# Performance work log

Measured on AMD Instinct MI355X. Metric: run time of the kernel, lower is better.

The kernel has to match this reference:

```python
import jax, jax.numpy as jnp
import numpy as np

BN_EPS = 1e-5

def _bn_relu(x, gamma, beta):
    # x: [E, B, F]; BatchNorm1d in training mode: batch stats over B, biased var
    mu = jnp.mean(x, axis=1, keepdims=True)
    var = jnp.mean(jnp.square(x - mu), axis=1, keepdims=True)
    y = gamma[:, None, :] * (x - mu) * jax.lax.rsqrt(var + BN_EPS) + beta[:, None, :]
    return jax.nn.relu(y)

def setup_inputs() -> dict:
    key = jax.random.key(0)
    ks = jax.random.split(key, 4)
    B, D, E, H1, H2, T = 32768, 1472, 8, 512, 256, 2
    s1 = (2.0 / D) ** 0.5
    s2 = (2.0 / H1) ** 0.5
    return {
        "x_deep": jax.random.normal(ks[0], (B, D), jnp.float32),
        "W1": jax.random.normal(ks[1], (E, D, H1), jnp.float32) * s1,
        "b1": jnp.zeros((E, H1), jnp.float32),
        "g1": jnp.ones((E, H1), jnp.float32),
        "be1": jnp.zeros((E, H1), jnp.float32),
        "W2": jax.random.normal(ks[2], (E, H1, H2), jnp.float32) * s2,
        "b2": jnp.zeros((E, H2), jnp.float32),
        "g2": jnp.ones((E, H2), jnp.float32),
        "be2": jnp.zeros((E, H2), jnp.float32),
        "Wg": jax.random.normal(ks[3], (T, D, E), jnp.float32) * s1,
        "bg": jnp.zeros((T, E), jnp.float32),
    }

def reference(x_deep, W1, b1, g1, be1, W2, b2, g2, be2, Wg, bg):
    # Experts: batched over expert dim E (replaces Python loop over nn.ModuleList)
    h = jnp.einsum('bd,edh->ebh', x_deep, W1) + b1[:, None, :]   # [E,B,H1]
    h = _bn_relu(h, g1, be1)                                     # dropout: identity (eval)
    h = jnp.einsum('ebh,ehk->ebk', h, W2) + b2[:, None, :]       # [E,B,H2]
    experts_out = _bn_relu(h, g2, be2)                           # [E,B,H2]
    # Gates: [T,B,E], softmax over experts
    gates = jax.nn.softmax(jnp.einsum('bd,tde->tbe', x_deep, Wg) + bg[:, None, :], axis=-1)
    # Combine: task_out[t] = reshape(experts_out * gate[...,None], [B, E*H2])
    task = experts_out[None, :, :, :] * jnp.transpose(gates, (0, 2, 1))[:, :, :, None]  # [T,E,B,H2]
    T, E, B, H2 = task.shape
    out = jnp.transpose(task, (0, 2, 1, 3)).reshape(T, B, E * H2)  # [T,B,E*H2]
    return out
```

## Files before the change

### kernel.cpp

```cpp
#include <hip/hip_runtime.h>
#include <cstdint>


typedef __attribute__((ext_vector_type(8))) __bf16 bf16x8;
typedef __attribute__((ext_vector_type(4))) float f32x4;

__device__ __forceinline__ unsigned short f2bf(float f) {
  unsigned int u = __float_as_uint(f);
  u += 0x7fffu + ((u >> 16) & 1u);
  return (unsigned short)(u >> 16);
}

__device__ __forceinline__ void async16(const void* g, void* l) {
  __builtin_amdgcn_global_load_lds((__attribute__((address_space(1))) unsigned int*)g,
                                   (__attribute__((address_space(3))) unsigned int*)l,
                                   16, 0, 0);
}

__global__ void convert_f32_bf16(const float* __restrict__ in,
                                 unsigned short* __restrict__ out, size_t n) {
  size_t i = ((size_t)blockIdx.x * blockDim.x + threadIdx.x) * 4;
  if (i + 3 < n) {
    float4 v = *(const float4*)(in + i);
    unsigned int w0 = (unsigned int)f2bf(v.x) | ((unsigned int)f2bf(v.y) << 16);
    unsigned int w1 = (unsigned int)f2bf(v.z) | ((unsigned int)f2bf(v.w) << 16);
    *(uint2*)(out + i) = make_uint2(w0, w1);
  }
}

__global__ void transpose_bf16(const float* __restrict__ W,
                               unsigned short* __restrict__ Wt, int D, int H) {
  __shared__ float tile[32][33];
  int e = blockIdx.z;
  int d0 = blockIdx.x * 32, h0 = blockIdx.y * 32;
  const float* We = W + (size_t)e * D * H;
  unsigned short* Wte = Wt + (size_t)e * D * H;
  int tx = threadIdx.x, ty = threadIdx.y;
#pragma unroll
  for (int i = 0; i < 4; ++i)
    tile[ty + i * 8][tx] = We[(size_t)(d0 + ty + i * 8) * H + h0 + tx];
  __syncthreads();
#pragma unroll
  for (int i = 0; i < 4; ++i)
    Wte[(size_t)(h0 + ty + i * 8) * D + d0 + tx] = f2bf(tile[tx][ty + i * 8]);
}

__global__ void transpose_wg(const float* __restrict__ Wg,
                             unsigned short* __restrict__ Wt, int D) {
  int idx = blockIdx.x * 256 + threadIdx.x;
  int te = idx / D, d = idx - te * D;
  int t = te >> 3, e = te & 7;
  Wt[(size_t)te * D + d] = f2bf(Wg[((size_t)t * D + d) * 8 + e]);
}

__global__ __launch_bounds__(512, 2) void gemm256(
    const unsigned short* __restrict__ A, int lda,
    const unsigned short* __restrict__ Bt,
    unsigned short* __restrict__ C, int ldc, int K,
    size_t aStrideE, size_t bStrideE, size_t cStrideE,
    float* __restrict__ sum, float* __restrict__ sq,
    int statStrideE, int statCols, int groupM, int GN) {
  __shared__ __attribute__((aligned(128))) char smem[131072];
  const int tid = threadIdx.x;
  const int lane = tid & 63;
  const int wid = tid >> 6;
  const int wm = wid & 1;
  const int wn = wid >> 1;
  const int e = blockIdx.z;

  int bx, by;
  if (groupM) {
    int bid = blockIdx.x;
    int cpx = (int)gridDim.x >> 3;
    int b2 = (bid & 7) * cpx + (bid >> 3);
    int gsize = groupM * GN;
    int gid = b2 / gsize;
    int rem = b2 - gid * gsize;
    bx = gid * groupM + rem % groupM;
    by = rem / groupM;
  } else {
    bx = blockIdx.x; by = blockIdx.y;
  }

  const unsigned short* Ae = A + (size_t)e * aStrideE + (size_t)bx * 256 * lda;
  const unsigned short* Be = Bt + (size_t)e * bStrideE + (size_t)by * 256 * K;

  const int srow = tid >> 2;
  const int scol = 8 * ((tid & 3) ^ ((tid >> 3) & 3));
  const unsigned short* gA = Ae + (size_t)srow * lda + scol;
  const unsigned short* gB = Be + (size_t)srow * K + scol;
  const size_t aRow128 = (size_t)128 * lda;
  const size_t bRow128 = (size_t)128 * K;
  char* ldsDst = smem + tid * 16;

  auto stageA = [&](int u) {
    char* d = ldsDst + (u & 3) * 32768;
    const unsigned short* g = gA + u * 32;
    async16(g, d);
    async16(g + aRow128, d + 8192);
  };
  auto stageB = [&](int u) {
    char* d = ldsDst + (u & 3) * 32768 + 16384;
    const unsigned short* g = gB + u * 32;
    async16(g, d);
    async16(g + bRow128, d + 8192);
  };

  const int mrow = lane & 15;
  const int kgb = ((lane >> 4) << 4) ^ (((mrow >> 1) & 3) << 4);
  const char* rdA = smem + (wm * 128 + mrow) * 64 + kgb;
  const char* rdB = smem + 16384 + (wn * 64 + mrow) * 64 + kgb;

  f32x4 acc[8][4] = {};
  const int NS = K >> 5;

  auto slab = [&](int u, bool st) {
    const char* pa = rdA + (u & 3) * 32768;
    const char* pb = rdB + (u & 3) * 32768;
    bf16x8 af[4], bfr[4];
#pragma unroll
    for (int i = 0; i < 4; ++i) af[i] = *(const bf16x8*)(pa + i * 1024);
#pragma unroll
    for (int j = 0; j < 4; ++j) bfr[j] = *(const bf16x8*)(pb + j * 1024);
    if (st) stageA(u + 2);
    __builtin_amdgcn_s_barrier();
    __builtin_amdgcn_s_setprio(1);
#pragma unroll
    for (int i = 0; i < 4; ++i)
#pragma unroll
      for (int j = 0; j < 4; ++j)
        acc[i][j] = __builtin_amdgcn_mfma_f32_16x16x32_bf16(af[i], bfr[j], acc[i][j], 0, 0, 0);
    __builtin_amdgcn_s_setprio(0);
    __builtin_amdgcn_s_barrier();
#pragma unroll
    for (int i = 0; i < 4; ++i) af[i] = *(const bf16x8*)(pa + (i + 4) * 1024);
    if (st) stageB(u + 2);
    __builtin_amdgcn_s_barrier();
    __builtin_amdgcn_s_setprio(1);
#pragma unroll
    for (int i = 0; i < 4; ++i)
#pragma unroll
      for (int j = 0; j < 4; ++j)
        acc[i + 4][j] = __builtin_amdgcn_mfma_f32_16x16x32_bf16(af[i], bfr[j], acc[i + 4][j], 0, 0, 0);
    __builtin_amdgcn_s_setprio(0);
  };

  stageA(0); stageB(0); stageA(1); stageB(1);
  asm volatile("s_waitcnt vmcnt(4)");
  __builtin_amdgcn_s_barrier();
  __builtin_amdgcn_sched_barrier(0);

  int u = 0;
  for (; u < NS - 2; ++u) {
    slab(u, true);
    asm volatile("s_waitcnt vmcnt(4)");
    __builtin_amdgcn_s_barrier();
    __builtin_amdgcn_sched_barrier(0);
  }
  slab(u, false); ++u;
  asm volatile("s_waitcnt vmcnt(0)");
  __builtin_amdgcn_s_barrier();
  __builtin_amdgcn_sched_barrier(0);
  slab(u, false);

  unsigned short* Ce = C + (size_t)e * cStrideE + (size_t)bx * 256 * ldc +
                       (size_t)by * 256;
  const int r0 = wm * 128 + (lane >> 4) * 4;
  const int c0 = wn * 64 + mrow;
#pragma unroll
  for (int i = 0; i < 8; ++i)
#pragma unroll
    for (int j = 0; j < 4; ++j)
#pragma unroll
      for (int r = 0; r < 4; ++r)
        Ce[(size_t)(r0 + i * 16 + r) * ldc + c0 + j * 16] = f2bf(acc[i][j][r]);

  float* se = sum + (size_t)e * statStrideE;
  float* qe = sq + (size_t)e * statStrideE;
#pragma unroll
  for (int j = 0; j < 4; ++j) {
    float s = 0.f, q = 0.f;
#pragma unroll
    for (int i = 0; i < 8; ++i)
#pragma unroll
      for (int r = 0; r < 4; ++r) {
        float v = acc[i][j][r];
        s += v;
        q = fmaf(v, v, q);
      }
    s += __shfl_xor(s, 16, 64); s += __shfl_xor(s, 32, 64);
    q += __shfl_xor(q, 16, 64); q += __shfl_xor(q, 32, 64);
    if ((lane >> 4) == 0) {
      int col = by * 256 + wn * 64 + j * 16 + mrow;
      if (col < statCols) {
        atomicAdd(&se[col], s);
        atomicAdd(&qe[col], q);
      }
    }
  }
}

__global__ void bn_coef(const float* __restrict__ sum, const float* __restrict__ sq,
                        const float* __restrict__ g, const float* __restrict__ be,
                        float* __restrict__ A, float* __restrict__ C, int n, float invB) {
  int i = blockIdx.x * blockDim.x + threadIdx.x;
  if (i < n) {
    float mean = sum[i] * invB;
    float var = sq[i] * invB - mean * mean;
    float a = g[i] * rsqrtf(var + 1e-5f);
    A[i] = a;
    C[i] = be[i] - mean * a;
  }
}

__global__ __launch_bounds__(256) void gates_mfma(
    const unsigned short* __restrict__ xb,
    const unsigned short* __restrict__ wgt,
    const float* __restrict__ bg,
    float* __restrict__ gates, int Bn) {
  const int lane = threadIdx.x & 63;
  const int w = threadIdx.x >> 6;
  const int row0 = blockIdx.x * 64 + w * 16;
  const int mrow = lane & 15, kseg = (lane >> 4) * 8;
  const unsigned short* pa = xb + (size_t)(row0 + mrow) * 1472 + kseg;
  const unsigned short* pb = wgt + (size_t)mrow * 1472 + kseg;
  f32x4 acc = {};
  bf16x8 a0 = *(const bf16x8*)pa, b0 = *(const bf16x8*)pb;
  for (int ks = 1; ks < 46; ++ks) {
    bf16x8 a1 = *(const bf16x8*)(pa + ks * 32);
    bf16x8 b1 = *(const bf16x8*)(pb + ks * 32);
    acc = __builtin_amdgcn_mfma_f32_16x16x32_bf16(a0, b0, acc, 0, 0, 0);
    a0 = a1; b0 = b1;
  }
  acc = __builtin_amdgcn_mfma_f32_16x16x32_bf16(a0, b0, acc, 0, 0, 0);
  const int c = lane & 15;
  const float bias = bg[c];
#pragma unroll
  for (int r = 0; r < 4; ++r) {
    float v = acc[r] + bias;
    float m = v;
    m = fmaxf(m, __shfl_xor(m, 1, 64));
    m = fmaxf(m, __shfl_xor(m, 2, 64));
    m = fmaxf(m, __shfl_xor(m, 4, 64));
    float p = expf(v - m);
    float s = p;
    s += __shfl_xor(s, 1, 64);
    s += __shfl_xor(s, 2, 64);
    s += __shfl_xor(s, 4, 64);
    int rowg = row0 + (lane >> 4) * 4 + r;
    gates[((size_t)(c >> 3) * Bn + rowg) * 8 + (c & 7)] = p / s;
  }
}

__global__ void bn_relu_inplace(unsigned short* __restrict__ h, const float* __restrict__ A,
                                const float* __restrict__ C) {
  int tid = blockIdx.x * blockDim.x + threadIdx.x;
  int r = tid >> 9, cb = tid & 511;
  int col = cb * 8;
  size_t i = (size_t)r * 4096 + col;
  uint4 v = *(const uint4*)(h + i);
  unsigned int w[4] = {v.x, v.y, v.z, v.w};
#pragma unroll
  for (int j = 0; j < 4; ++j) {
    float f0 = __uint_as_float(w[j] << 16);
    float f1 = __uint_as_float(w[j] & 0xffff0000u);
    float y0 = fmaxf(fmaf(A[col + 2 * j], f0, C[col + 2 * j]), 0.f);
    float y1 = fmaxf(fmaf(A[col + 2 * j + 1], f1, C[col + 2 * j + 1]), 0.f);
    w[j] = (unsigned int)f2bf(y0) | ((unsigned int)f2bf(y1) << 16);
  }
  *(uint4*)(h + i) = make_uint4(w[0], w[1], w[2], w[3]);
}

__global__ void combine(const unsigned short* __restrict__ h2,
                        const float* __restrict__ A, const float* __restrict__ C,
                        const float* __restrict__ gates,
                        float* __restrict__ out, int Bn) {
  int b = blockIdx.x;
  int c = threadIdx.x * 8;
  int e = c >> 8;
  uint4 v = *(const uint4*)(h2 + (size_t)b * 2048 + c);
  unsigned int w[4] = {v.x, v.y, v.z, v.w};
  float y[8];
#pragma unroll
  for (int j = 0; j < 4; ++j) {
    float f0 = __uint_as_float(w[j] << 16);
    float f1 = __uint_as_float(w[j] & 0xffff0000u);
    y[2 * j]     = fmaxf(fmaf(A[c + 2 * j], f0, C[c + 2 * j]), 0.f);
    y[2 * j + 1] = fmaxf(fmaf(A[c + 2 * j + 1], f1, C[c + 2 * j + 1]), 0.f);
  }
  float g0 = gates[(size_t)b * 8 + e];
  float g1 = gates[((size_t)Bn + b) * 8 + e];
  float4* o0 = (float4*)(out + (size_t)b * 2048 + c);
  float4* o1 = (float4*)(out + ((size_t)Bn + b) * 2048 + c);
  o0[0] = make_float4(y[0] * g0, y[1] * g0, y[2] * g0, y[3] * g0);
  o0[1] = make_float4(y[4] * g0, y[5] * g0, y[6] * g0, y[7] * g0);
  o1[0] = make_float4(y[0] * g1, y[1] * g1, y[2] * g1, y[3] * g1);
  o1[1] = make_float4(y[4] * g1, y[5] * g1, y[6] * g1, y[7] * g1);
}

extern "C" void kernel_launch(void* const* d_in, const int* in_sizes, int n_in,
                              void* d_out, int out_size, void* d_ws, size_t ws_size,
                              hipStream_t stream) {
  const int B = 32768, D = 1472, E = 8, H1 = 512, H2 = 256;
  const int N1 = E * H1;
  const float* x   = (const float*)d_in[0];
  const float* W1  = (const float*)d_in[1];
  const float* g1  = (const float*)d_in[3];
  const float* be1 = (const float*)d_in[4];
  const float* W2  = (const float*)d_in[5];
  const float* g2  = (const float*)d_in[7];
  const float* be2 = (const float*)d_in[8];
  const float* Wg  = (const float*)d_in[9];
  const float* bg  = (const float*)d_in[10];
  float* out = (float*)d_out;

  char* p = (char*)d_ws;
  unsigned short* x_b = (unsigned short*)p; p += (size_t)B * D * 2;
  unsigned short* W1t = (unsigned short*)p; p += (size_t)N1 * D * 2;
  unsigned short* Wgt = (unsigned short*)p; p += (size_t)16 * D * 2;
  unsigned short* W2t = (unsigned short*)p; p += (size_t)E * H2 * H1 * 2;
  unsigned short* h1b = (unsigned short*)p; p += (size_t)B * N1 * 2;
  unsigned short* h2b = (unsigned short*)p; p += (size_t)B * E * H2 * 2;
  float* gatesBuf = (float*)p; p += (size_t)2 * B * 8 * 4;
  float* sum1 = (float*)p; p += (size_t)N1 * 4;
  float* sq1  = (float*)p; p += (size_t)N1 * 4;
  float* sum2 = (float*)p; p += (size_t)E * H2 * 4;
  float* sq2  = (float*)p; p += (size_t)E * H2 * 4;
  float* A1   = (float*)p; p += (size_t)N1 * 4;
  float* C1   = (float*)p; p += (size_t)N1 * 4;
  float* A2   = (float*)p; p += (size_t)E * H2 * 4;
  float* C2   = (float*)p; p += (size_t)E * H2 * 4;

  hipMemsetAsync(sum1, 0, (size_t)(2 * N1 + 2 * E * H2) * 4, stream);

  convert_f32_bf16<<<(unsigned)((size_t)B * D / 1024), 256, 0, stream>>>(
      x, x_b, (size_t)B * D);
  transpose_bf16<<<dim3(D / 32, H1 / 32, E), dim3(32, 8), 0, stream>>>(W1, W1t, D, H1);
  transpose_wg<<<16 * D / 256, 256, 0, stream>>>(Wg, Wgt, D);
  transpose_bf16<<<dim3(H1 / 32, H2 / 32, E), dim3(32, 8), 0, stream>>>(W2, W2t, H1, H2);

  gemm256<<<dim3(128 * 16), 512, 0, stream>>>(
      x_b, D, W1t, h1b, N1, D, (size_t)0, (size_t)0, (size_t)0,
      sum1, sq1, 0, N1, 16, 16);

  bn_coef<<<N1 / 256, 256, 0, stream>>>(sum1, sq1, g1, be1, A1, C1, N1, 1.f / B);
  gates_mfma<<<B / 64, 256, 0, stream>>>(x_b, Wgt, bg, gatesBuf, B);
  bn_relu_inplace<<<(unsigned)((size_t)B * 512 / 256), 256, 0, stream>>>(h1b, A1, C1);

  gemm256<<<dim3(B / 256, 1, E), 512, 0, stream>>>(
      h1b, N1, W2t, h2b, E * H2, H1,
      (size_t)H1, (size_t)H1 * H2, (size_t)H2,
      sum2, sq2, H2, H2, 0, 0);

  bn_coef<<<E * H2 / 256, 256, 0, stream>>>(sum2, sq2, g2, be2, A2, C2, E * H2, 1.f / B);

  combine<<<B, 256, 0, stream>>>(h2b, A2, C2, gatesBuf, out, B);
}
```

Before: 1.458 ms.

## Fuse BN1+ReLU into second expert GEMM's A-operand load path

Removes the separate in-place BN+ReLU pass over the 32768x4096 bf16 hidden activation and applies the affine+ReLU while staging A tiles into LDS in a new dedicated GEMM2 kernel with a double-buffered register-load pipeline. This saves a full read and write of h1. The new kernel uses a shallower 2-stage pipeline with synchronous register loads for A instead of the 4-stage async pipeline, which may expose more memory latency. The generic GEMM loses its per-expert stride parameters.

Measured after the change: 1.351 ms. -7.4%, faster.

```diff
diff --git a/kernel.cpp b/kernel.cpp
--- a/kernel.cpp
+++ b/kernel.cpp
@@ -57,33 +57,26 @@
     const unsigned short* __restrict__ A, int lda,
     const unsigned short* __restrict__ Bt,
     unsigned short* __restrict__ C, int ldc, int K,
-    size_t aStrideE, size_t bStrideE, size_t cStrideE,
     float* __restrict__ sum, float* __restrict__ sq,
-    int statStrideE, int statCols, int groupM, int GN) {
+    int statCols, int groupM, int GN) {
   __shared__ __attribute__((aligned(128))) char smem[131072];
   const int tid = threadIdx.x;
   const int lane = tid & 63;
   const int wid = tid >> 6;
   const int wm = wid & 1;
   const int wn = wid >> 1;
-  const int e = blockIdx.z;
-
-  int bx, by;
-  if (groupM) {
-    int bid = blockIdx.x;
-    int cpx = (int)gridDim.x >> 3;
-    int b2 = (bid & 7) * cpx + (bid >> 3);
-    int gsize = groupM * GN;
-    int gid = b2 / gsize;
-    int rem = b2 - gid * gsize;
-    bx = gid * groupM + rem % groupM;
-    by = rem / groupM;
-  } else {
-    bx = blockIdx.x; by = blockIdx.y;
-  }
-
-  const unsigned short* Ae = A + (size_t)e * aStrideE + (size_t)bx * 256 * lda;
-  const unsigned short* Be = Bt + (size_t)e * bStrideE + (size_t)by * 256 * K;
+
+  int bid = blockIdx.x;
+  int cpx = (int)gridDim.x >> 3;
+  int b2 = (bid & 7) * cpx + (bid >> 3);
+  int gsize = groupM * GN;
+  int gid = b2 / gsize;
+  int rem = b2 - gid * gsize;
+  int bx = gid * groupM + rem % groupM;
+  int by = rem / groupM;
+
+  const unsigned short* Ae = A + (size_t)bx * 256 * lda;
+  const unsigned short* Be = Bt + (size_t)by * 256 * K;
 
   const int srow = tid >> 2;
   const int scol = 8 * ((tid & 3) ^ ((tid >> 3) & 3));
@@ -163,8 +156,7 @@
   __builtin_amdgcn_sched_barrier(0);
   slab(u, false);
 
-  unsigned short* Ce = C + (size_t)e * cStrideE + (size_t)bx * 256 * ldc +
-                       (size_t)by * 256;
+  unsigned short* Ce = C + (size_t)bx * 256 * ldc + (size_t)by * 256;
   const int r0 = wm * 128 + (lane >> 4) * 4;
   const int c0 = wn * 64 + mrow;
 #pragma unroll
@@ -175,8 +167,6 @@
       for (int r = 0; r < 4; ++r)
         Ce[(size_t)(r0 + i * 16 + r) * ldc + c0 + j * 16] = f2bf(acc[i][j][r]);
 
-  float* se = sum + (size_t)e * statStrideE;
-  float* qe = sq + (size_t)e * statStrideE;
 #pragma unroll
   for (int j = 0; j < 4; ++j) {
     float s = 0.f, q = 0.f;
@@ -193,9 +183,136 @@
     if ((lane >> 4) == 0) {
       int col = by * 256 + wn * 64 + j * 16 + mrow;
       if (col < statCols) {
-        atomicAdd(&se[col], s);
-        atomicAdd(&qe[col], q);
+        atomicAdd(&sum[col], s);
+        atomicAdd(&sq[col], q);
       }
+    }
+  }
+}
+
+__global__ __launch_bounds__(512) void gemm2_fused(
+    const unsigned short* __restrict__ H1,
+    const float* __restrict__ A1, const float* __restrict__ C1,
+    const unsigned short* __restrict__ W2t,
+    unsigned short* __restrict__ H2,
+    float* __restrict__ sum, float* __restrict__ sq) {
+  __shared__ __attribute__((aligned(128))) char smem[2][32768];
+  const int tid = threadIdx.x;
+  const int lane = tid & 63;
+  const int wid = tid >> 6;
+  const int wm = wid & 1;
+  const int wn = wid >> 1;
+  const int e = blockIdx.z;
+  const int bx = blockIdx.x;
+
+  const unsigned short* Ae = H1 + (size_t)bx * 256 * 4096 + e * 512;
+  const unsigned short* Be = W2t + (size_t)e * 256 * 512;
+
+  const int srow = tid >> 2;
+  const int scol = 8 * ((tid & 3) ^ ((tid >> 3) & 3));
+  const unsigned short* gA = Ae + (size_t)srow * 4096 + scol;
+  const unsigned short* gB = Be + (size_t)srow * 512 + scol;
+  const size_t aRow128 = (size_t)128 * 4096;
+  const size_t bRow128 = (size_t)128 * 512;
+  const float* a1p = A1 + e * 512 + scol;
+  const float* c1p = C1 + e * 512 + scol;
+
+  auto bnrelu = [&](uint4 v, int kc) -> uint4 {
+    unsigned int w[4] = {v.x, v.y, v.z, v.w};
+    unsigned int o[4];
+#pragma unroll
+    for (int j = 0; j < 4; ++j) {
+      float f0 = __uint_as_float(w[j] << 16);
+      float f1 = __uint_as_float(w[j] & 0xffff0000u);
+      float y0 = fmaxf(fmaf(a1p[kc + 2 * j], f0, c1p[kc + 2 * j]), 0.f);
+      float y1 = fmaxf(fmaf(a1p[kc + 2 * j + 1], f1, c1p[kc + 2 * j + 1]), 0.f);
+      o[j] = (unsigned int)f2bf(y0) | ((unsigned int)f2bf(y1) << 16);
+    }
+    return make_uint4(o[0], o[1], o[2], o[3]);
+  };
+
+  const int mrow = lane & 15;
+  const int kgb = ((lane >> 4) << 4) ^ (((mrow >> 1) & 3) << 4);
+  const int rdAo = (wm * 128 + mrow) * 64 + kgb;
+  const int rdBo = 16384 + (wn * 64 + mrow) * 64 + kgb;
+
+  f32x4 acc[8][4] = {};
+
+  {
+    uint4 va0 = *(const uint4*)(gA);
+    uint4 va1 = *(const uint4*)(gA + aRow128);
+    async16(gB, smem[0] + tid * 16 + 16384);
+    async16(gB + bRow128, smem[0] + tid * 16 + 16384 + 8192);
+    uint4 t0 = bnrelu(va0, 0), t1 = bnrelu(va1, 0);
+    *(uint4*)(smem[0] + tid * 16) = t0;
+    *(uint4*)(smem[0] + tid * 16 + 8192) = t1;
+  }
+  __syncthreads();
+
+  for (int u = 0; u < 16; ++u) {
+    const int slot = u & 1, nslot = slot ^ 1;
+    uint4 va0, va1;
+    if (u < 15) {
+      va0 = *(const uint4*)(gA + (u + 1) * 32);
+      va1 = *(const uint4*)(gA + (u + 1) * 32 + aRow128);
+      async16(gB + (u + 1) * 32, smem[nslot] + tid * 16 + 16384);
+      async16(gB + (u + 1) * 32 + bRow128, smem[nslot] + tid * 16 + 16384 + 8192);
+    }
+    {
+      const char* pa = smem[slot] + rdAo;
+      const char* pb = smem[slot] + rdBo;
+      bf16x8 af[8], bfr[4];
+#pragma unroll
+      for (int i = 0; i < 8; ++i) af[i] = *(const bf16x8*)(pa + i * 1024);
+#pragma unroll
+      for (int j = 0; j < 4; ++j) bfr[j] = *(const bf16x8*)(pb + j * 1024);
+      __builtin_amdgcn_s_setprio(1);
+#pragma unroll
+      for (int i = 0; i < 8; ++i)
+#pragma unroll
+        for (int j = 0; j < 4; ++j)
+          acc[i][j] = __builtin_amdgcn_mfma_f32_16x16x32_bf16(af[i], bfr[j], acc[i][j], 0, 0, 0);
+      __builtin_amdgcn_s_setprio(0);
+    }
+    if (u < 15) {
+      uint4 t0 = bnrelu(va0, (u + 1) * 32);
+      uint4 t1 = bnrelu(va1, (u + 1) * 32);
+      *(uint4*)(smem[nslot] + tid * 16) = t0;
+      *(uint4*)(smem[nslot] + tid * 16 + 8192) = t1;
+    }
+    __syncthreads();
+  }
+
+  unsigned short* Ce = H2 + (size_t)bx * 256 * 2048 + e * 256;
+  const int r0 = wm * 128 + (lane >> 4) * 4;
+  const int c0 = wn * 64 + mrow;
+#pragma unroll
+  for (int i = 0; i < 8; ++i)
+#pragma unroll
+    for (int j = 0; j < 4; ++j)
+#pragma unroll
+      for (int r = 0; r < 4; ++r)
+        Ce[(size_t)(r0 + i * 16 + r) * 2048 + c0 + j * 16] = f2bf(acc[i][j][r]);
+
+  float* se = sum + (size_t)e * 256;
+  float* qe = sq + (size_t)e * 256;
+#pragma unroll
+  for (int j = 0; j < 4; ++j) {
+    float s = 0.f, q = 0.f;
+#pragma unroll
+    for (int i = 0; i < 8; ++i)
+#pragma unroll
+      for (int r = 0; r < 4; ++r) {
+        float v = acc[i][j][r];
+        s += v;
+        q = fmaf(v, v, q);
+      }
+    s += __shfl_xor(s, 16, 64); s += __shfl_xor(s, 32, 64);
+    q += __shfl_xor(q, 16, 64); q += __shfl_xor(q, 32, 64);
+    if ((lane >> 4) == 0) {
+      int col = wn * 64 + j * 16 + mrow;
+      atomicAdd(&se[col], s);
+      atomicAdd(&qe[col], q);
     }
   }
 }
@@ -252,25 +369,6 @@
   }
 }
 
-__global__ void bn_relu_inplace(unsigned short* __restrict__ h, const float* __restrict__ A,
-                                const float* __restrict__ C) {
-  int tid = blockIdx.x * blockDim.x + threadIdx.x;
-  int r = tid >> 9, cb = tid & 511;
-  int col = cb * 8;
-  size_t i = (size_t)r * 4096 + col;
-  uint4 v = *(const uint4*)(h + i);
-  unsigned int w[4] = {v.x, v.y, v.z, v.w};
-#pragma unroll
-  for (int j = 0; j < 4; ++j) {
-    float f0 = __uint_as_float(w[j] << 16);
-    float f1 = __uint_as_float(w[j] & 0xffff0000u);
-    float y0 = fmaxf(fmaf(A[col + 2 * j], f0, C[col + 2 * j]), 0.f);
-    float y1 = fmaxf(fmaf(A[col + 2 * j + 1], f1, C[col + 2 * j + 1]), 0.f);
-    w[j] = (unsigned int)f2bf(y0) | ((unsigned int)f2bf(y1) << 16);
-  }
-  *(uint4*)(h + i) = make_uint4(w[0], w[1], w[2], w[3]);
-}
-
 __global__ void combine(const unsigned short* __restrict__ h2,
                         const float* __restrict__ A, const float* __restrict__ C,
                         const float* __restrict__ gates,
@@ -340,17 +438,13 @@
   transpose_bf16<<<dim3(H1 / 32, H2 / 32, E), dim3(32, 8), 0, stream>>>(W2, W2t, H1, H2);
 
   gemm256<<<dim3(128 * 16), 512, 0, stream>>>(
-      x_b, D, W1t, h1b, N1, D, (size_t)0, (size_t)0, (size_t)0,
-      sum1, sq1, 0, N1, 16, 16);
+      x_b, D, W1t, h1b, N1, D, sum1, sq1, N1, 16, 16);
 
   bn_coef<<<N1 / 256, 256, 0, stream>>>(sum1, sq1, g1, be1, A1, C1, N1, 1.f / B);
   gates_mfma<<<B / 64, 256, 0, stream>>>(x_b, Wgt, bg, gatesBuf, B);
-  bn_relu_inplace<<<(unsigned)((size_t)B * 512 / 256), 256, 0, stream>>>(h1b, A1, C1);
-
-  gemm256<<<dim3(B / 256, 1, E), 512, 0, stream>>>(
-      h1b, N1, W2t, h2b, E * H2, H1,
-      (size_t)H1, (size_t)H1 * H2, (size_t)H2,
-      sum2, sq2, H2, H2, 0, 0);
+
+  gemm2_fused<<<dim3(B / 256, 1, E), 512, 0, stream>>>(
+      h1b, A1, C1, W2t, h2b, sum2, sq2);
 
   bn_coef<<<E * H2 / 256, 256, 0, stream>>>(sum2, sq2, g2, be2, A2, C2, E * H2, 1.f / B);
 
```
